# Optimization experiments

Measured on AMD Instinct MI355X. Metric: run time of the kernel, lower is better.

Reference implementation:

```python
import jax, jax.numpy as jnp
import numpy as np

R = 100        # voxel grid resolution per axis
N = 200000     # number of active (non-empty) voxels
K = 3          # kernel size
CIN = 64
COUT = 64
NOFF = K ** 3 - 1  # 26 non-center offsets


def _build_maps():
    # Mirrors mapping_cuda: per kernel offset, find (input_row, output_row) pairs
    # such that coords[input] == coords[output] + offset (submanifold conv,
    # output coords == input coords).
    rng = np.random.default_rng(0)
    lin = rng.choice(R ** 3, size=N, replace=False)
    coords = np.stack(np.unravel_index(lin, (R, R, R)), axis=1)  # [N,3]
    lut = np.full(R ** 3, -1, dtype=np.int64)
    lut[lin] = np.arange(N)
    offs = [(dx, dy, dz) for dx in (-1, 0, 1) for dy in (-1, 0, 1)
            for dz in (-1, 0, 1) if (dx, dy, dz) != (0, 0, 0)]
    ins, outs = [], []
    for d in offs:
        tgt = coords - np.asarray(d)              # output coord receiving input i
        valid = np.all((tgt >= 0) & (tgt < R), axis=1)
        idx_i = np.nonzero(valid)[0]
        tlin = np.ravel_multi_index(tgt[valid].T, (R, R, R))
        j = lut[tlin]
        hit = j >= 0
        ins.append(idx_i[hit].astype(np.int32))
        outs.append(j[hit].astype(np.int32))
    P = max(len(a) for a in ins)
    imap = np.full((NOFF, P), -1, dtype=np.int32)
    omap = np.full((NOFF, P), -1, dtype=np.int32)
    for k, (a, b) in enumerate(zip(ins, outs)):
        imap[k, :len(a)] = a
        omap[k, :len(b)] = b
    return jnp.asarray(imap), jnp.asarray(omap)


def setup_inputs() -> dict:
    key = jax.random.key(0)
    kf, kw = jax.random.split(key)
    feats = jax.random.normal(kf, (N, CIN), dtype=jnp.float32)
    # reset_parameters: uniform(-stdv, stdv), stdv = 1/sqrt(out_channels * K^3)
    stdv = 1.0 / float(np.sqrt(COUT * K ** 3))
    kernel = jax.random.uniform(kw, (K ** 3, CIN, COUT), dtype=jnp.float32,
                                minval=-stdv, maxval=stdv)
    imap, omap = _build_maps()
    return {"feats": feats, "kernel": kernel, "imap": imap, "omap": omap}


def reference(feats, kernel, imap, omap):
    # Submanifold sparse 3D conv: gather -> per-offset GEMM -> scatter-add.
    K3 = kernel.shape[0]
    c = K3 // 2  # center offset: identity neighbor map
    w_nc = jnp.concatenate([kernel[:c], kernel[c + 1:]], axis=0)  # [26,Cin,Cout]
    mask = imap >= 0                                   # [26,P]
    gath = feats[jnp.where(mask, imap, 0)] * mask[..., None]   # [26,P,Cin]
    y = jnp.einsum('kpc,kco->kpo', gath, w_nc)         # [26,P,Cout]
    out = feats @ kernel[c]                            # center contribution [N,Cout]
    oi = jnp.where(mask, omap, 0).reshape(-1)          # masked rows add zeros at row 0
    out = out.at[oi].add(y.reshape(-1, y.shape[-1]))
    return out
```

## Files before the change

kernel.cpp:

```cpp
#include <hip/hip_runtime.h>


#define CIN 64
#define COUT 64
#define TR 32
#define NOFF 26

typedef short bf16x8 __attribute__((ext_vector_type(8)));
typedef unsigned short ushort8 __attribute__((ext_vector_type(8)));
typedef float f32x4 __attribute__((ext_vector_type(4)));

__device__ inline unsigned short bfbits(float f) {
    unsigned u = __builtin_bit_cast(unsigned, f);
    u += 0x7fffu + ((u >> 16) & 1u);
    return (unsigned short)(u >> 16);
}

__device__ inline int kk_of_item(int i) {
    return (i == 26) ? 13 : 26 - (i < 13 ? i : i + 1);
}

__global__ __launch_bounds__(256) void prep_feats(const float* __restrict__ f,
                                                  unsigned short* __restrict__ fb,
                                                  int n) {
    const int i8 = (blockIdx.x * 256 + threadIdx.x) * 8;
    if (i8 >= n) return;
    const float4 v0 = *(const float4*)(f + i8);
    const float4 v1 = *(const float4*)(f + i8 + 4);
    union { unsigned short u[8]; bf16x8 v; } r;
    r.u[0] = bfbits(v0.x); r.u[1] = bfbits(v0.y);
    r.u[2] = bfbits(v0.z); r.u[3] = bfbits(v0.w);
    r.u[4] = bfbits(v1.x); r.u[5] = bfbits(v1.y);
    r.u[6] = bfbits(v1.z); r.u[7] = bfbits(v1.w);
    *(bf16x8*)(fb + i8) = r.v;
}

__global__ __launch_bounds__(256) void prep_wt(const float* __restrict__ W,
                                               unsigned short* __restrict__ Wt) {
    const int k = blockIdx.x;
    for (int idx = threadIdx.x; idx < CIN * COUT; idx += 256) {
        const int c = idx >> 6, o = idx & 63;
        const int q = c >> 3, e = c & 7;
        Wt[((k * 64 + o) * 64) + (((q ^ (o & 7)) << 3) + e)] =
            bfbits(W[(k * 64 + c) * 64 + o]);
    }
}

__global__ __launch_bounds__(256) void prep_tab_init(int4* __restrict__ tab4, int n4) {
    const int i = blockIdx.x * 256 + threadIdx.x;
    if (i < n4) tab4[i] = make_int4(-1, -1, -1, -1);
}

__global__ __launch_bounds__(256) void prep_tab(const int* __restrict__ imap,
                                                const int* __restrict__ omap,
                                                int P, int nt,
                                                int* __restrict__ tab) {
    const int p = blockIdx.x * 256 + threadIdx.x;
    const int m = blockIdx.y;
    if (p >= P) return;
    const int iv = imap[(size_t)m * P + p];
    if (iv < 0) return;
    tab[((size_t)m * nt + (iv >> 5)) * TR + (iv & 31)] = omap[(size_t)m * P + p];
}

__global__ __launch_bounds__(256) void spconv_v5(
    const unsigned short* __restrict__ fb,
    const unsigned short* __restrict__ wt,
    const int* __restrict__ tab,
    float* __restrict__ out, int N, int nt)
{
    __shared__ unsigned short wbuf[2][4096];

    const int tid = threadIdx.x, w = tid >> 6, lane = tid & 63;
    const int col = lane & 15, grp = lane >> 4;
    const int t = blockIdx.x * 4 + w;
    const bool vt = (t < nt);
    const int tt = vt ? t : (nt - 1);
    const int r0 = t * TR;

    auto tabload = [&](int j) -> int {
        const int jc = (j < 26) ? j : 25;
        return 0;
    };
    (void)tabload;

#define TABLOAD(j, s) tab[((size_t)((j) < 26 ? (j) : 25) * nt + tt) * TR + (s) * 16 + col]
#define RESOLVE(j, s, tv) \
    ((!vt || (j) > 26) ? -1 : ((j) == 26 ? ((r0 + (s)*16 + col < N) ? r0 + (s)*16 + col : -1) : (tv)))

    int sv_c[2], sv_n[2], tv2[2], tv3[2];
#pragma unroll
    for (int s = 0; s < 2; ++s) {
        sv_c[s] = RESOLVE(0, s, TABLOAD(0, s));
        sv_n[s] = RESOLVE(1, s, TABLOAD(1, s));
        tv2[s] = TABLOAD(2, s);
        tv3[s] = TABLOAD(3, s);
    }

    bf16x8 a_cur[2][2], a_nx[2][2];
#pragma unroll
    for (int s = 0; s < 2; ++s) {
        const int sc = (sv_c[s] < 0) ? 0 : sv_c[s];
        const bf16x8* fp = (const bf16x8*)(fb + (size_t)sc * 64 + grp * 8);
        a_cur[s][0] = fp[0];
        a_cur[s][1] = fp[4];
    }

    {
        const unsigned short* wk = wt + kk_of_item(0) * 4096;
        const ushort8 wl0 = *(const ushort8*)(wk + tid * 8);
        const ushort8 wl1 = *(const ushort8*)(wk + 2048 + tid * 8);
        *(ushort8*)(&wbuf[0][tid * 8]) = wl0;
        *(ushort8*)(&wbuf[0][2048 + tid * 8]) = wl1;
    }
    asm volatile("s_waitcnt lgkmcnt(0)" ::: "memory");
    __builtin_amdgcn_s_barrier();

    f32x4 acc[2][4];
#pragma unroll
    for (int s = 0; s < 2; ++s)
#pragma unroll
        for (int ot = 0; ot < 4; ++ot) acc[s][ot] = {0.f, 0.f, 0.f, 0.f};

    for (int it = 0; it < 27; ++it) {
        const int itn = (it < 26) ? it + 1 : 26;
        const unsigned short* wkn = wt + kk_of_item(itn) * 4096;
        const ushort8 wl0 = *(const ushort8*)(wkn + tid * 8);
        const ushort8 wl1 = *(const ushort8*)(wkn + 2048 + tid * 8);

#pragma unroll
        for (int s = 0; s < 2; ++s) {
            const int sc = (sv_n[s] < 0) ? 0 : sv_n[s];
            const bf16x8* fp = (const bf16x8*)(fb + (size_t)sc * 64 + grp * 8);
            a_nx[s][0] = fp[0];
            a_nx[s][1] = fp[4];
        }

        int sv_nn[2];
#pragma unroll
        for (int s = 0; s < 2; ++s) {
            sv_nn[s] = RESOLVE(it + 2, s, tv2[s]);
            tv2[s] = tv3[s];
            tv3[s] = TABLOAD(it + 4, s);
        }

#pragma unroll
        for (int s = 0; s < 2; ++s)
            if (sv_c[s] < 0) { a_cur[s][0] = (bf16x8)0; a_cur[s][1] = (bf16x8)0; }

        const unsigned short* cb = wbuf[it & 1];
#pragma unroll
        for (int ot = 0; ot < 4; ++ot) {
            const int o = ot * 16 + col;
            const bf16x8 b0 = *(const bf16x8*)(cb + o * 64 + ((grp ^ (col & 7)) << 3));
            const bf16x8 b1 = *(const bf16x8*)(cb + o * 64 + (((4 + grp) ^ (col & 7)) << 3));
#pragma unroll
            for (int s = 0; s < 2; ++s) {
                acc[s][ot] = __builtin_amdgcn_mfma_f32_16x16x32_bf16(a_cur[s][0], b0, acc[s][ot], 0, 0, 0);
                acc[s][ot] = __builtin_amdgcn_mfma_f32_16x16x32_bf16(a_cur[s][1], b1, acc[s][ot], 0, 0, 0);
            }
        }

        unsigned short* nb = wbuf[(it + 1) & 1];
        *(ushort8*)(&nb[tid * 8]) = wl0;
        *(ushort8*)(&nb[2048 + tid * 8]) = wl1;

        asm volatile("s_waitcnt lgkmcnt(0)" ::: "memory");
        __builtin_amdgcn_s_barrier();

#pragma unroll
        for (int s = 0; s < 2; ++s) {
            sv_c[s] = sv_n[s];
            sv_n[s] = sv_nn[s];
            a_cur[s][0] = a_nx[s][0];
            a_cur[s][1] = a_nx[s][1];
        }
    }

    if (vt) {
#pragma unroll
        for (int s = 0; s < 2; ++s)
#pragma unroll
            for (int ot = 0; ot < 4; ++ot) {
                const f32x4 cv = acc[s][ot];
#pragma unroll
                for (int reg = 0; reg < 4; ++reg) {
                    const int r = r0 + s * 16 + grp * 4 + reg;
                    if (r < N) out[(size_t)r * 64 + ot * 16 + col] = cv[reg];
                }
            }
    }
#undef TABLOAD
#undef RESOLVE
}

template <int MODE>
__global__ __launch_bounds__(256) void spconv_fb(
    const float* __restrict__ feats, const float* __restrict__ W,
    const int* __restrict__ imap, const int* __restrict__ omap,
    float* __restrict__ out, int npairs)
{
    __shared__ float4 wt4[16 * 64];
    const int tid = threadIdx.x, koff = blockIdx.y;
    const float* Wk;
    const int* im = nullptr; const int* om = nullptr;
    if (MODE == 0) Wk = W + 13 * (CIN * COUT);
    else {
        const int kk = (koff < 13) ? koff : koff + 1;
        Wk = W + (size_t)kk * (CIN * COUT);
        im = imap + (size_t)koff * npairs; om = omap + (size_t)koff * npairs;
    }
    float* wts = (float*)wt4;
    for (int idx = tid; idx < CIN * COUT; idx += 256) {
        const int c = idx >> 6, o = idx & 63;
        wts[((c >> 2) * 64 + o) * 4 + (c & 3)] = Wk[idx];
    }
    __syncthreads();
    const int o = tid & 63, w = tid >> 6;
    const int base = blockIdx.x * 256 + w * 64;
    const float4* f4p = (const float4*)feats;
    for (int n = 0; n < 64; ++n) {
        const int p = base + n;
        if (p >= npairs) break;
        int i, j;
        if (MODE == 0) { i = p; j = p; }
        else { i = im[p]; if (i < 0) continue; j = om[p]; }
        i = __builtin_amdgcn_readfirstlane(i);
        float a = 0.f;
#pragma unroll
        for (int c4 = 0; c4 < 16; ++c4) {
            const float4 f = f4p[(size_t)i * 16 + c4];
            const float4 wv = wt4[c4 * 64 + o];
            a += f.x * wv.x + f.y * wv.y + f.z * wv.z + f.w * wv.w;
        }
        if (MODE == 0) out[(size_t)j * COUT + o] = a;
        else atomicAdd(&out[(size_t)j * COUT + o], a);
    }
}

extern "C" void kernel_launch(void* const* d_in, const int* in_sizes, int n_in,
                              void* d_out, int out_size, void* d_ws, size_t ws_size,
                              hipStream_t stream) {
    const float* feats = (const float*)d_in[0];
    const float* W     = (const float*)d_in[1];
    const int* imap    = (const int*)d_in[2];
    const int* omap    = (const int*)d_in[3];
    float* out         = (float*)d_out;

    const int N = in_sizes[0] / CIN;
    const int P = in_sizes[2] / NOFF;
    const int nt = (N + TR - 1) / TR;

    const size_t fb_bytes  = (size_t)N * 64 * sizeof(unsigned short);
    const size_t wt_bytes  = 27 * 64 * 64 * sizeof(unsigned short);
    const size_t tab_bytes = (size_t)NOFF * nt * TR * sizeof(int);

    if (ws_size < fb_bytes + wt_bytes + tab_bytes) {
        dim3 blk(256);
        dim3 gc((N + 255) / 256, 1);
        spconv_fb<0><<<gc, blk, 0, stream>>>(feats, W, nullptr, nullptr, out, N);
        dim3 go((P + 255) / 256, NOFF);
        spconv_fb<1><<<go, blk, 0, stream>>>(feats, W, imap, omap, out, P);
        return;
    }

    unsigned short* fbp = (unsigned short*)d_ws;
    unsigned short* Wt  = (unsigned short*)((char*)d_ws + fb_bytes);
    int* tab            = (int*)((char*)d_ws + fb_bytes + wt_bytes);

    const int nf = N * 64;
    prep_feats<<<(nf / 8 + 255) / 256, 256, 0, stream>>>(feats, fbp, nf);
    prep_wt<<<27, 256, 0, stream>>>(W, Wt);
    const int n4 = (int)(tab_bytes / 16);
    prep_tab_init<<<(n4 + 255) / 256, 256, 0, stream>>>((int4*)tab, n4);
    prep_tab<<<dim3((P + 255) / 256, NOFF), 256, 0, stream>>>(imap, omap, P, nt, tab);

    spconv_v5<<<(nt + 3) / 4, 256, 0, stream>>>(fbp, Wt, tab, out, N, nt);
}
```

Before: 95.47 us.

## Double rows per wave and replace masking with a zero sentinel feature row

Each wave now covers 64 output rows instead of 32, so each weight tile staged in shared memory is reused across twice as many MFMA operations and the grid has half as many blocks. Empty neighbor slots now point at an extra all-zero feature row at index N instead of -1, which removes the per-iteration clamp and zeroing branches. The table prefetch depth drops from two to one iteration, and MFMA sections get raised scheduling priority. The cost is more accumulator and A-operand registers per lane (possible occupancy loss), fewer blocks for latency hiding, and an extra memset of the sentinel row.

New measurement: 106.4 us. 11.4% more time.

```diff
diff --git a/kernel.cpp b/kernel.cpp
--- a/kernel.cpp
+++ b/kernel.cpp
@@ -3,7 +3,7 @@
 
 #define CIN 64
 #define COUT 64
-#define TR 32
+#define TR 64
 #define NOFF 26
 
 typedef short bf16x8 __attribute__((ext_vector_type(8)));
@@ -17,7 +17,7 @@
 }
 
 __device__ inline int kk_of_item(int i) {
-    return (i == 26) ? 13 : 26 - (i < 13 ? i : i + 1);
+    return (i >= 26) ? 13 : 26 - (i < 13 ? i : i + 1);
 }
 
 __global__ __launch_bounds__(256) void prep_feats(const float* __restrict__ f,
@@ -46,9 +46,10 @@
     }
 }
 
-__global__ __launch_bounds__(256) void prep_tab_init(int4* __restrict__ tab4, int n4) {
+__global__ __launch_bounds__(256) void prep_tab_init(int4* __restrict__ tab4,
+                                                     int n4, int N) {
     const int i = blockIdx.x * 256 + threadIdx.x;
-    if (i < n4) tab4[i] = make_int4(-1, -1, -1, -1);
+    if (i < n4) tab4[i] = make_int4(N, N, N, N);
 }
 
 __global__ __launch_bounds__(256) void prep_tab(const int* __restrict__ imap,
@@ -60,10 +61,10 @@
     if (p >= P) return;
     const int iv = imap[(size_t)m * P + p];
     if (iv < 0) return;
-    tab[((size_t)m * nt + (iv >> 5)) * TR + (iv & 31)] = omap[(size_t)m * P + p];
-}
-
-__global__ __launch_bounds__(256) void spconv_v5(
+    tab[((size_t)m * nt + (iv >> 6)) * TR + (iv & 63)] = omap[(size_t)m * P + p];
+}
+
+__global__ __launch_bounds__(256) void spconv_v6(
     const unsigned short* __restrict__ fb,
     const unsigned short* __restrict__ wt,
     const int* __restrict__ tab,
@@ -74,34 +75,38 @@
     const int tid = threadIdx.x, w = tid >> 6, lane = tid & 63;
     const int col = lane & 15, grp = lane >> 4;
     const int t = blockIdx.x * 4 + w;
-    const bool vt = (t < nt);
-    const int tt = vt ? t : (nt - 1);
+    const int tt = (t < nt) ? t : (nt - 1);
     const int r0 = t * TR;
-
-    auto tabload = [&](int j) -> int {
-        const int jc = (j < 26) ? j : 25;
-        return 0;
+    const size_t tstep = (size_t)nt * TR;
+
+    const int* tb0 = tab + (size_t)tt * TR + col;
+
+    auto resolve = [&](int j, const int* tv, int* sv) {
+#pragma unroll
+        for (int s = 0; s < 4; ++s) {
+            int v;
+            if (j < 26) v = tv[s];
+            else if (j == 26) { const int r = r0 + s * 16 + col; v = (r < N) ? r : N; }
+            else v = N;
+            sv[s] = v;
+        }
     };
-    (void)tabload;
-
-#define TABLOAD(j, s) tab[((size_t)((j) < 26 ? (j) : 25) * nt + tt) * TR + (s) * 16 + col]
-#define RESOLVE(j, s, tv) \
-    ((!vt || (j) > 26) ? -1 : ((j) == 26 ? ((r0 + (s)*16 + col < N) ? r0 + (s)*16 + col : -1) : (tv)))
-
-    int sv_c[2], sv_n[2], tv2[2], tv3[2];
-#pragma unroll
-    for (int s = 0; s < 2; ++s) {
-        sv_c[s] = RESOLVE(0, s, TABLOAD(0, s));
-        sv_n[s] = RESOLVE(1, s, TABLOAD(1, s));
-        tv2[s] = TABLOAD(2, s);
-        tv3[s] = TABLOAD(3, s);
-    }
-
-    bf16x8 a_cur[2][2], a_nx[2][2];
-#pragma unroll
-    for (int s = 0; s < 2; ++s) {
-        const int sc = (sv_c[s] < 0) ? 0 : sv_c[s];
-        const bf16x8* fp = (const bf16x8*)(fb + (size_t)sc * 64 + grp * 8);
+
+    int t0[4], t1[4], tv2[4];
+#pragma unroll
+    for (int s = 0; s < 4; ++s) {
+        t0[s]  = tb0[s * 16];
+        t1[s]  = (tb0 + tstep)[s * 16];
+        tv2[s] = (tb0 + 2 * tstep)[s * 16];
+    }
+    int sv_c[4], sv_n[4];
+    resolve(0, t0, sv_c);
+    resolve(1, t1, sv_n);
+
+    bf16x8 a_cur[4][2], a_nx[4][2];
+#pragma unroll
+    for (int s = 0; s < 4; ++s) {
+        const bf16x8* fp = (const bf16x8*)(fb + (size_t)sv_c[s] * 64 + grp * 8);
         a_cur[s][0] = fp[0];
         a_cur[s][1] = fp[4];
     }
@@ -116,50 +121,47 @@
     asm volatile("s_waitcnt lgkmcnt(0)" ::: "memory");
     __builtin_amdgcn_s_barrier();
 
-    f32x4 acc[2][4];
-#pragma unroll
-    for (int s = 0; s < 2; ++s)
+    f32x4 acc[4][4];
+#pragma unroll
+    for (int s = 0; s < 4; ++s)
 #pragma unroll
         for (int ot = 0; ot < 4; ++ot) acc[s][ot] = {0.f, 0.f, 0.f, 0.f};
 
     for (int it = 0; it < 27; ++it) {
-        const int itn = (it < 26) ? it + 1 : 26;
-        const unsigned short* wkn = wt + kk_of_item(itn) * 4096;
+        const unsigned short* wkn = wt + kk_of_item(it + 1) * 4096;
         const ushort8 wl0 = *(const ushort8*)(wkn + tid * 8);
         const ushort8 wl1 = *(const ushort8*)(wkn + 2048 + tid * 8);
 
 #pragma unroll
-        for (int s = 0; s < 2; ++s) {
-            const int sc = (sv_n[s] < 0) ? 0 : sv_n[s];
-            const bf16x8* fp = (const bf16x8*)(fb + (size_t)sc * 64 + grp * 8);
+        for (int s = 0; s < 4; ++s) {
+            const bf16x8* fp = (const bf16x8*)(fb + (size_t)sv_n[s] * 64 + grp * 8);
             a_nx[s][0] = fp[0];
             a_nx[s][1] = fp[4];
         }
 
-        int sv_nn[2];
-#pragma unroll
-        for (int s = 0; s < 2; ++s) {
-            sv_nn[s] = RESOLVE(it + 2, s, tv2[s]);
-            tv2[s] = tv3[s];
-            tv3[s] = TABLOAD(it + 4, s);
-        }
-
-#pragma unroll
-        for (int s = 0; s < 2; ++s)
-            if (sv_c[s] < 0) { a_cur[s][0] = (bf16x8)0; a_cur[s][1] = (bf16x8)0; }
+        int sv_nn[4];
+        resolve(it + 2, tv2, sv_nn);
+        {
+            const int j3 = (it + 3 < 26) ? it + 3 : 25;
+            const int* tb3 = tb0 + (size_t)j3 * tstep;
+#pragma unroll
+            for (int s = 0; s < 4; ++s) tv2[s] = tb3[s * 16];
+        }
 
         const unsigned short* cb = wbuf[it & 1];
+        __builtin_amdgcn_s_setprio(1);
 #pragma unroll
         for (int ot = 0; ot < 4; ++ot) {
             const int o = ot * 16 + col;
             const bf16x8 b0 = *(const bf16x8*)(cb + o * 64 + ((grp ^ (col & 7)) << 3));
             const bf16x8 b1 = *(const bf16x8*)(cb + o * 64 + (((4 + grp) ^ (col & 7)) << 3));
 #pragma unroll
-            for (int s = 0; s < 2; ++s) {
+            for (int s = 0; s < 4; ++s) {
                 acc[s][ot] = __builtin_amdgcn_mfma_f32_16x16x32_bf16(a_cur[s][0], b0, acc[s][ot], 0, 0, 0);
                 acc[s][ot] = __builtin_amdgcn_mfma_f32_16x16x32_bf16(a_cur[s][1], b1, acc[s][ot], 0, 0, 0);
             }
         }
+        __builtin_amdgcn_s_setprio(0);
 
         unsigned short* nb = wbuf[(it + 1) & 1];
         *(ushort8*)(&nb[tid * 8]) = wl0;
@@ -169,7 +171,7 @@
         __builtin_amdgcn_s_barrier();
 
 #pragma unroll
-        for (int s = 0; s < 2; ++s) {
+        for (int s = 0; s < 4; ++s) {
             sv_c[s] = sv_n[s];
             sv_n[s] = sv_nn[s];
             a_cur[s][0] = a_nx[s][0];
@@ -177,21 +179,17 @@
         }
     }
 
-    if (vt) {
-#pragma unroll
-        for (int s = 0; s < 2; ++s)
-#pragma unroll
-            for (int ot = 0; ot < 4; ++ot) {
-                const f32x4 cv = acc[s][ot];
-#pragma unroll
-                for (int reg = 0; reg < 4; ++reg) {
-                    const int r = r0 + s * 16 + grp * 4 + reg;
-                    if (r < N) out[(size_t)r * 64 + ot * 16 + col] = cv[reg];
-                }
+#pragma unroll
+    for (int s = 0; s < 4; ++s)
+#pragma unroll
+        for (int ot = 0; ot < 4; ++ot) {
+            const f32x4 cv = acc[s][ot];
+#pragma unroll
+            for (int reg = 0; reg < 4; ++reg) {
+                const int r = r0 + s * 16 + grp * 4 + reg;
+                if (r < N) out[(size_t)r * 64 + ot * 16 + col] = cv[reg];
             }
-    }
-#undef TABLOAD
-#undef RESOLVE
+        }
 }
 
 template <int MODE>
@@ -251,7 +249,7 @@
     const int P = in_sizes[2] / NOFF;
     const int nt = (N + TR - 1) / TR;
 
-    const size_t fb_bytes  = (size_t)N * 64 * sizeof(unsigned short);
+    const size_t fb_bytes  = (size_t)(N + 1) * 64 * sizeof(unsigned short);
     const size_t wt_bytes  = 27 * 64 * 64 * sizeof(unsigned short);
     const size_t tab_bytes = (size_t)NOFF * nt * TR * sizeof(int);
 
@@ -270,10 +268,11 @@
 
     const int nf = N * 64;
     prep_feats<<<(nf / 8 + 255) / 256, 256, 0, stream>>>(feats, fbp, nf);
+    hipMemsetAsync(fbp + (size_t)N * 64, 0, 128, stream);
     prep_wt<<<27, 256, 0, stream>>>(W, Wt);
     const int n4 = (int)(tab_bytes / 16);
-    prep_tab_init<<<(n4 + 255) / 256, 256, 0, stream>>>((int4*)tab, n4);
+    prep_tab_init<<<(n4 + 255) / 256, 256, 0, stream>>>((int4*)tab, n4, N);
     prep_tab<<<dim3((P + 255) / 256, NOFF), 256, 0, stream>>>(imap, omap, P, nt, tab);
 
-    spconv_v5<<<(nt + 3) / 4, 256, 0, stream>>>(fbp, Wt, tab, out, N, nt);
-}
+    spconv_v6<<<(nt + 3) / 4, 256, 0, stream>>>(fbp, Wt, tab, out, N, nt);
+}
```

## Deepen feature prefetch, use zero-row sentinel, remap blocks across XCDs

Applied to the files above, without the earlier changes.

Missing neighbours now point to a zero-filled sentinel row instead of -1, and the center offset becomes a 27th table slice. This removes the per-iteration RESOLVE and zero-masking logic from the main loop. Feature gathers are prefetched two iterations ahead with triple-buffered registers, and MFMA sections get raised wave priority. Block indices are remapped so consecutive tiles land on the same XCD for L2 locality. The costs are more VGPRs (launch bounds now request 4 blocks), a larger table-init pass and an extra memset.

New measurement: 107.7 us. +12.8%, slower.

```diff
diff --git a/kernel.cpp b/kernel.cpp
--- a/kernel.cpp
+++ b/kernel.cpp
@@ -17,7 +17,7 @@
 }
 
 __device__ inline int kk_of_item(int i) {
-    return (i == 26) ? 13 : 26 - (i < 13 ? i : i + 1);
+    return (i >= 26) ? 13 : 26 - (i < 13 ? i : i + 1);
 }
 
 __global__ __launch_bounds__(256) void prep_feats(const float* __restrict__ f,
@@ -46,9 +46,22 @@
     }
 }
 
-__global__ __launch_bounds__(256) void prep_tab_init(int4* __restrict__ tab4, int n4) {
-    const int i = blockIdx.x * 256 + threadIdx.x;
-    if (i < n4) tab4[i] = make_int4(-1, -1, -1, -1);
+__global__ __launch_bounds__(256) void prep_tab_init(int* __restrict__ tab,
+                                                     int nt, int N) {
+    const size_t i4 = ((size_t)blockIdx.x * 256 + threadIdx.x) * 4;
+    const size_t total = (size_t)27 * nt * TR;
+    if (i4 >= total) return;
+    const size_t mstep = (size_t)nt * TR;
+    int4 v;
+    int* vp = (int*)&v;
+#pragma unroll
+    for (int e = 0; e < 4; ++e) {
+        const size_t l = i4 + e;
+        const int m = (int)(l / mstep);
+        const int r = (int)(l - (size_t)m * mstep);
+        vp[e] = (m == 26 && r < N) ? r : N;
+    }
+    *(int4*)(tab + i4) = v;
 }
 
 __global__ __launch_bounds__(256) void prep_tab(const int* __restrict__ imap,
@@ -63,47 +76,45 @@
     tab[((size_t)m * nt + (iv >> 5)) * TR + (iv & 31)] = omap[(size_t)m * P + p];
 }
 
-__global__ __launch_bounds__(256) void spconv_v5(
+__global__ __launch_bounds__(256, 4) void spconv_v7(
     const unsigned short* __restrict__ fb,
     const unsigned short* __restrict__ wt,
     const int* __restrict__ tab,
-    float* __restrict__ out, int N, int nt)
+    float* __restrict__ out, int N, int nt, int nwg)
 {
     __shared__ unsigned short wbuf[2][4096];
 
     const int tid = threadIdx.x, w = tid >> 6, lane = tid & 63;
     const int col = lane & 15, grp = lane >> 4;
-    const int t = blockIdx.x * 4 + w;
-    const bool vt = (t < nt);
-    const int tt = vt ? t : (nt - 1);
+
+    const int orig = blockIdx.x;
+    const int q = nwg >> 3, r8 = nwg & 7;
+    const int xcd = orig & 7, k = orig >> 3;
+    const int sb = (xcd < r8 ? xcd * (q + 1) : r8 * (q + 1) + (xcd - r8) * q) + k;
+
+    const int t = sb * 4 + w;
+    const int tt = (t < nt) ? t : (nt - 1);
     const int r0 = t * TR;
-
-    auto tabload = [&](int j) -> int {
-        const int jc = (j < 26) ? j : 25;
-        return 0;
-    };
-    (void)tabload;
-
-#define TABLOAD(j, s) tab[((size_t)((j) < 26 ? (j) : 25) * nt + tt) * TR + (s) * 16 + col]
-#define RESOLVE(j, s, tv) \
-    ((!vt || (j) > 26) ? -1 : ((j) == 26 ? ((r0 + (s)*16 + col < N) ? r0 + (s)*16 + col : -1) : (tv)))
-
-    int sv_c[2], sv_n[2], tv2[2], tv3[2];
+    const size_t tstep = (size_t)nt * TR;
+    const int* tb = tab + (size_t)tt * TR + col;
+
+#define TAB(j, s) tb[(size_t)((j) < 27 ? (j) : 26) * tstep + (s) * 16]
+
+    int sv1[2], sv2[2], tvA[2], tvB[2];
+    bf16x8 a0[2][2], a1[2][2], a2[2][2];
 #pragma unroll
     for (int s = 0; s < 2; ++s) {
-        sv_c[s] = RESOLVE(0, s, TABLOAD(0, s));
-        sv_n[s] = RESOLVE(1, s, TABLOAD(1, s));
-        tv2[s] = TABLOAD(2, s);
-        tv3[s] = TABLOAD(3, s);
-    }
-
-    bf16x8 a_cur[2][2], a_nx[2][2];
-#pragma unroll
-    for (int s = 0; s < 2; ++s) {
-        const int sc = (sv_c[s] < 0) ? 0 : sv_c[s];
-        const bf16x8* fp = (const bf16x8*)(fb + (size_t)sc * 64 + grp * 8);
-        a_cur[s][0] = fp[0];
-        a_cur[s][1] = fp[4];
+        const int sv0 = TAB(0, s);
+        sv1[s] = TAB(1, s);
+        sv2[s] = TAB(2, s);
+        tvA[s] = TAB(3, s);
+        tvB[s] = TAB(4, s);
+        const bf16x8* fp = (const bf16x8*)(fb + (size_t)sv0 * 64 + grp * 8);
+        a0[s][0] = fp[0];
+        a0[s][1] = fp[4];
+        const bf16x8* fq = (const bf16x8*)(fb + (size_t)sv1[s] * 64 + grp * 8);
+        a1[s][0] = fq[0];
+        a1[s][1] = fq[4];
     }
 
     {
@@ -123,32 +134,27 @@
         for (int ot = 0; ot < 4; ++ot) acc[s][ot] = {0.f, 0.f, 0.f, 0.f};
 
     for (int it = 0; it < 27; ++it) {
-        const int itn = (it < 26) ? it + 1 : 26;
-        const unsigned short* wkn = wt + kk_of_item(itn) * 4096;
+        const unsigned short* wkn = wt + kk_of_item(it + 1) * 4096;
         const ushort8 wl0 = *(const ushort8*)(wkn + tid * 8);
         const ushort8 wl1 = *(const ushort8*)(wkn + 2048 + tid * 8);
 
 #pragma unroll
         for (int s = 0; s < 2; ++s) {
-            const int sc = (sv_n[s] < 0) ? 0 : sv_n[s];
-            const bf16x8* fp = (const bf16x8*)(fb + (size_t)sc * 64 + grp * 8);
-            a_nx[s][0] = fp[0];
-            a_nx[s][1] = fp[4];
-        }
-
-        int sv_nn[2];
+            const bf16x8* fp = (const bf16x8*)(fb + (size_t)sv2[s] * 64 + grp * 8);
+            a2[s][0] = fp[0];
+            a2[s][1] = fp[4];
+        }
+
+        int svn[2];
 #pragma unroll
         for (int s = 0; s < 2; ++s) {
-            sv_nn[s] = RESOLVE(it + 2, s, tv2[s]);
-            tv2[s] = tv3[s];
-            tv3[s] = TABLOAD(it + 4, s);
-        }
-
-#pragma unroll
-        for (int s = 0; s < 2; ++s)
-            if (sv_c[s] < 0) { a_cur[s][0] = (bf16x8)0; a_cur[s][1] = (bf16x8)0; }
+            svn[s] = tvA[s];
+            tvA[s] = tvB[s];
+            tvB[s] = TAB(it + 5, s);
+        }
 
         const unsigned short* cb = wbuf[it & 1];
+        __builtin_amdgcn_s_setprio(1);
 #pragma unroll
         for (int ot = 0; ot < 4; ++ot) {
             const int o = ot * 16 + col;
@@ -156,10 +162,11 @@
             const bf16x8 b1 = *(const bf16x8*)(cb + o * 64 + (((4 + grp) ^ (col & 7)) << 3));
 #pragma unroll
             for (int s = 0; s < 2; ++s) {
-                acc[s][ot] = __builtin_amdgcn_mfma_f32_16x16x32_bf16(a_cur[s][0], b0, acc[s][ot], 0, 0, 0);
-                acc[s][ot] = __builtin_amdgcn_mfma_f32_16x16x32_bf16(a_cur[s][1], b1, acc[s][ot], 0, 0, 0);
+                acc[s][ot] = __builtin_amdgcn_mfma_f32_16x16x32_bf16(a0[s][0], b0, acc[s][ot], 0, 0, 0);
+                acc[s][ot] = __builtin_amdgcn_mfma_f32_16x16x32_bf16(a0[s][1], b1, acc[s][ot], 0, 0, 0);
             }
         }
+        __builtin_amdgcn_s_setprio(0);
 
         unsigned short* nb = wbuf[(it + 1) & 1];
         *(ushort8*)(&nb[tid * 8]) = wl0;
@@ -170,28 +177,24 @@
 
 #pragma unroll
         for (int s = 0; s < 2; ++s) {
-            sv_c[s] = sv_n[s];
-            sv_n[s] = sv_nn[s];
-            a_cur[s][0] = a_nx[s][0];
-            a_cur[s][1] = a_nx[s][1];
-        }
-    }
-
-    if (vt) {
-#pragma unroll
-        for (int s = 0; s < 2; ++s)
-#pragma unroll
-            for (int ot = 0; ot < 4; ++ot) {
-                const f32x4 cv = acc[s][ot];
-#pragma unroll
-                for (int reg = 0; reg < 4; ++reg) {
-                    const int r = r0 + s * 16 + grp * 4 + reg;
-                    if (r < N) out[(size_t)r * 64 + ot * 16 + col] = cv[reg];
-                }
+            a0[s][0] = a1[s][0]; a0[s][1] = a1[s][1];
+            a1[s][0] = a2[s][0]; a1[s][1] = a2[s][1];
+            sv2[s] = svn[s];
+        }
+    }
+
+#pragma unroll
+    for (int s = 0; s < 2; ++s)
+#pragma unroll
+        for (int ot = 0; ot < 4; ++ot) {
+            const f32x4 cv = acc[s][ot];
+#pragma unroll
+            for (int reg = 0; reg < 4; ++reg) {
+                const int rr = r0 + s * 16 + grp * 4 + reg;
+                if (rr < N) out[(size_t)rr * 64 + ot * 16 + col] = cv[reg];
             }
-    }
-#undef TABLOAD
-#undef RESOLVE
+        }
+#undef TAB
 }
 
 template <int MODE>
@@ -251,9 +254,9 @@
     const int P = in_sizes[2] / NOFF;
     const int nt = (N + TR - 1) / TR;
 
-    const size_t fb_bytes  = (size_t)N * 64 * sizeof(unsigned short);
+    const size_t fb_bytes  = (size_t)(N + 1) * 64 * sizeof(unsigned short);
     const size_t wt_bytes  = 27 * 64 * 64 * sizeof(unsigned short);
-    const size_t tab_bytes = (size_t)NOFF * nt * TR * sizeof(int);
+    const size_t tab_bytes = (size_t)27 * nt * TR * sizeof(int);
 
     if (ws_size < fb_bytes + wt_bytes + tab_bytes) {
         dim3 blk(256);
@@ -270,10 +273,12 @@
 
     const int nf = N * 64;
     prep_feats<<<(nf / 8 + 255) / 256, 256, 0, stream>>>(feats, fbp, nf);
+    hipMemsetAsync(fbp + (size_t)N * 64, 0, 128, stream);
     prep_wt<<<27, 256, 0, stream>>>(W, Wt);
-    const int n4 = (int)(tab_bytes / 16);
-    prep_tab_init<<<(n4 + 255) / 256, 256, 0, stream>>>((int4*)tab, n4);
+    const size_t tot4 = (size_t)27 * nt * TR / 4;
+    prep_tab_init<<<(int)((tot4 + 255) / 256), 256, 0, stream>>>(tab, nt, N);
     prep_tab<<<dim3((P + 255) / 256, NOFF), 256, 0, stream>>>(imap, omap, P, nt, tab);
 
-    spconv_v5<<<(nt + 3) / 4, 256, 0, stream>>>(fbp, Wt, tab, out, N, nt);
-}
+    const int nwg = (nt + 3) / 4;
+    spconv_v7<<<nwg, 256, 0, stream>>>(fbp, Wt, tab, out, N, nt, nwg);
+}
```
